# Kernel optimization log

Hardware: AMD Instinct MI355X
Metric: run time of the kernel (lower is better)

Reference implementation:

```python
import jax, jax.numpy as jnp
import numpy as np

IN_DIM = 512
NUM_HEADS = 8
KD = IN_DIM // 2   # 256
VD = IN_DIM        # 512
NEG = -1e9


def setup_inputs() -> dict:
    key = jax.random.key(0)
    k0, k1, k2, k3, k4 = jax.random.split(key, 5)
    B, C, H, W = 2, IN_DIM, 64, 64
    s = lambda fan_in: 1.0 / np.sqrt(fan_in)
    return {
        "X": jax.random.normal(k0, (B, C, H, W), dtype=jnp.float32),
        "Wq": jax.random.normal(k1, (IN_DIM, KD), dtype=jnp.float32) * s(IN_DIM),
        "Wk": jax.random.normal(k2, (IN_DIM, KD), dtype=jnp.float32) * s(IN_DIM),
        "Wv": jax.random.normal(k3, (IN_DIM, VD), dtype=jnp.float32) * s(IN_DIM),
        "Wo": jax.random.normal(k4, (VD, IN_DIM), dtype=jnp.float32) * s(VD),
    }


def reference(X, Wq, Wk, Wv, Wo):
    B, C, H, W = X.shape
    S = H * W
    x = jnp.transpose(X, (0, 2, 3, 1)).reshape(B, S, C)  # [B,S,C]
    dk = KD // NUM_HEADS
    dv = VD // NUM_HEADS
    # projections + head split -> [B,h,S,d]
    q = (x @ Wq).reshape(B, S, NUM_HEADS, dk).transpose(0, 2, 1, 3)
    k = (x @ Wk).reshape(B, S, NUM_HEADS, dk).transpose(0, 2, 1, 3)
    v = (x @ Wv).reshape(B, S, NUM_HEADS, dv).transpose(0, 2, 1, 3)
    q = q * (dk ** -0.5)
    logits = jnp.einsum('bhqd,bhkd->bhqk', q, k)
    bias = NEG * jnp.triu(jnp.ones((S, S), dtype=logits.dtype), 1)  # causal
    weights = jax.nn.softmax(logits + bias, axis=-1)
    out = weights @ v                                  # [B,h,S,dv]
    out = out.transpose(0, 2, 1, 3).reshape(B, S, VD)  # merge heads
    out = out @ Wo
    return out.reshape(B, H, W, C)
```

## Files before the change

### kernel.cpp

```cpp
#include <hip/hip_runtime.h>
#include <hip/hip_bf16.h>
#include <math.h>

#define BATCH 2
#define CH 512
#define SEQ 4096
#define KDIM 256
#define VDIM 512
#define NHEADS 8
#define DK 32
#define DV 64

typedef unsigned short u16;
typedef unsigned int u32;
typedef __attribute__((ext_vector_type(8))) short bf16x8;
typedef __attribute__((ext_vector_type(4))) float f32x4;

__device__ __forceinline__ u16 f2bf(float f) {
    u32 x = __float_as_uint(f);
    u32 r = (x + 0x7fffu + ((x >> 16) & 1u)) >> 16;
    return (u16)r;
}
__device__ __forceinline__ u16 f2bf_fast(float f) {
    return (u16)((__float_as_uint(f) + 0x8000u) >> 16);
}
__device__ __forceinline__ u32 pack2f(float lo, float hi) {
    return (u32)f2bf_fast(lo) | (((__float_as_uint(hi) + 0x8000u) >> 16) << 16);
}

#define QSCALE (0.17677669529663687f * 1.4426950408889634f)


__global__ __launch_bounds__(256) void prep(
    const float* __restrict__ X,
    const float* __restrict__ Wq, const float* __restrict__ Wk,
    const float* __restrict__ Wv, const float* __restrict__ Wo,
    u16* __restrict__ Xb16, u16* __restrict__ Wall, u16* __restrict__ WoT)
{
    __shared__ u16 T[64 * 72];
    const int bid = blockIdx.x;
    const int t = threadIdx.x;
    const int tr = t >> 4;
    const int tc4 = (t & 15) * 4;

    const float* src; u16* dst;
    int src_row0, src_col0, src_pitch, dst_row0, dst_col0, dst_pitch;
    float scale = 1.0f;

    if (bid < 1024) {
        const int b = bid >> 9, rem = bid & 511;
        const int st = rem >> 3, ct = rem & 7;
        src = X + (size_t)b * CH * SEQ;
        src_row0 = ct * 64; src_col0 = st * 64; src_pitch = SEQ;
        dst = Xb16 + (size_t)b * SEQ * CH;
        dst_row0 = st * 64; dst_col0 = ct * 64; dst_pitch = CH;
    } else if (bid < 1152) {
        const int r = bid - 1024;
        const int nt = r >> 3, ct = r & 7;
        if (nt < 4)      { src = Wq; src_col0 = nt * 64;       src_pitch = KDIM; scale = QSCALE; }
        else if (nt < 8) { src = Wk; src_col0 = (nt - 4) * 64; src_pitch = KDIM; }
        else             { src = Wv; src_col0 = (nt - 8) * 64; src_pitch = VDIM; }
        src_row0 = ct * 64;
        dst = Wall; dst_row0 = nt * 64; dst_col0 = ct * 64; dst_pitch = 512;
    } else {
        const int r = bid - 1152;
        const int kt = r >> 3, nt = r & 7;
        src = Wo; src_row0 = kt * 64; src_col0 = nt * 64; src_pitch = 512;
        dst = WoT; dst_row0 = nt * 64; dst_col0 = kt * 64; dst_pitch = 512;
    }

#pragma unroll
    for (int j = 0; j < 4; ++j) {
        const int row = j * 16 + tr;
        const float4 v = *reinterpret_cast<const float4*>(
            &src[(size_t)(src_row0 + row) * src_pitch + src_col0 + tc4]);
        T[(tc4 + 0) * 72 + row] = f2bf(v.x * scale);
        T[(tc4 + 1) * 72 + row] = f2bf(v.y * scale);
        T[(tc4 + 2) * 72 + row] = f2bf(v.z * scale);
        T[(tc4 + 3) * 72 + row] = f2bf(v.w * scale);
    }
    __syncthreads();
#pragma unroll
    for (int j = 0; j < 4; ++j) {
        const int orow = j * 16 + tr;
        const ushort4 o = *reinterpret_cast<ushort4*>(&T[orow * 72 + tc4]);
        *reinterpret_cast<ushort4*>(
            &dst[(size_t)(dst_row0 + orow) * dst_pitch + dst_col0 + tc4]) = o;
    }
}

__global__ __launch_bounds__(256, 2) void qkv3(
    const u16* __restrict__ Xb16, const u16* __restrict__ Wall,
    u16* __restrict__ Qh, u16* __restrict__ Kh, u16* __restrict__ Vh)
{
    __shared__ __align__(16) u16 As[2][128 * 40];
    __shared__ __align__(16) u16 Bs[2][128 * 40];
    const int tid = threadIdx.x;
    const int wv = tid >> 6, lane = tid & 63;
    const int c = lane & 15, quad = lane >> 4;
    const int wm = wv & 1, wn = wv >> 1;
    const int m0 = blockIdx.x * 128;
    const int ny = blockIdx.y;
    const int n0 = ny * 128;

    u16* Y; int N, nbase;
    if (ny < 2)      { Y = Qh; N = KDIM; nbase = 0; }
    else if (ny < 4) { Y = Kh; N = KDIM; nbase = 256; }
    else             { Y = Vh; N = VDIM; nbase = 512; }

    const int srow = tid >> 1, scol = (tid & 1) * 16;

    f32x4 acc[4][4];
#pragma unroll
    for (int i = 0; i < 4; ++i)
#pragma unroll
        for (int g = 0; g < 4; ++g) acc[i][g] = (f32x4){0.f, 0.f, 0.f, 0.f};

    uint4 ar0, ar1, br0, br1;
    auto ld = [&](int k0) {
        const uint4* ap = reinterpret_cast<const uint4*>(
            &Xb16[(size_t)(m0 + srow) * 512 + k0 + scol]);
        ar0 = ap[0]; ar1 = ap[1];
        const uint4* bp = reinterpret_cast<const uint4*>(
            &Wall[(size_t)(n0 + srow) * 512 + k0 + scol]);
        br0 = bp[0]; br1 = bp[1];
    };
    auto stage = [&](int buf) {
        uint4* ad = reinterpret_cast<uint4*>(&As[buf][srow * 40 + scol]);
        ad[0] = ar0; ad[1] = ar1;
        uint4* bd = reinterpret_cast<uint4*>(&Bs[buf][srow * 40 + scol]);
        bd[0] = br0; bd[1] = br1;
    };

    ld(0);
    stage(0);
    ld(32);

    for (int i = 0; i < 16; ++i) {
        const int cur = i & 1;
        __syncthreads();
        stage(cur ^ 1);
        const int k0n = (i + 2 < 16) ? (i + 2) * 32 : 15 * 32;
        ld(k0n);
        bf16x8 af[4], bf_[4];
#pragma unroll
        for (int j = 0; j < 4; ++j) {
            af[j] = *reinterpret_cast<bf16x8*>(
                &As[cur][(wm * 64 + 16 * j + c) * 40 + quad * 8]);
            bf_[j] = *reinterpret_cast<bf16x8*>(
                &Bs[cur][(wn * 64 + 16 * j + c) * 40 + quad * 8]);
        }
#pragma unroll
        for (int j = 0; j < 4; ++j)
#pragma unroll
            for (int g = 0; g < 4; ++g)
                acc[j][g] = __builtin_amdgcn_mfma_f32_16x16x32_bf16(
                    af[j], bf_[g], acc[j][g], 0, 0, 0);
    }
#pragma unroll
    for (int j = 0; j < 4; ++j)
#pragma unroll
        for (int r = 0; r < 4; ++r) {
            const int row = m0 + wm * 64 + 16 * j + quad * 4 + r;
            const int col = n0 - nbase + wn * 64 + c;
#pragma unroll
            for (int g = 0; g < 4; ++g)
                Y[(size_t)row * N + col + 16 * g] = f2bf(acc[j][g][r]);
        }
}

__global__ __launch_bounds__(256, 2) void oproj3(
    const u16* __restrict__ A, const u16* __restrict__ WoT,
    float* __restrict__ Out)
{
    __shared__ __align__(16) u16 As[2][128 * 40];
    __shared__ __align__(16) u16 Bs[2][128 * 40];
    const int tid = threadIdx.x;
    const int wv = tid >> 6, lane = tid & 63;
    const int c = lane & 15, quad = lane >> 4;
    const int wm = wv & 1, wn = wv >> 1;
    const int m0 = blockIdx.x * 128;
    const int n0 = blockIdx.y * 128;

    const int srow = tid >> 1, scol = (tid & 1) * 16;

    f32x4 acc[4][4];
#pragma unroll
    for (int i = 0; i < 4; ++i)
#pragma unroll
        for (int g = 0; g < 4; ++g) acc[i][g] = (f32x4){0.f, 0.f, 0.f, 0.f};

    uint4 ar0, ar1, br0, br1;
    auto ld = [&](int k0) {
        const uint4* ap = reinterpret_cast<const uint4*>(
            &A[(size_t)(m0 + srow) * 512 + k0 + scol]);
        ar0 = ap[0]; ar1 = ap[1];
        const uint4* bp = reinterpret_cast<const uint4*>(
            &WoT[(size_t)(n0 + srow) * 512 + k0 + scol]);
        br0 = bp[0]; br1 = bp[1];
    };
    auto stage = [&](int buf) {
        uint4* ad = reinterpret_cast<uint4*>(&As[buf][srow * 40 + scol]);
        ad[0] = ar0; ad[1] = ar1;
        uint4* bd = reinterpret_cast<uint4*>(&Bs[buf][srow * 40 + scol]);
        bd[0] = br0; bd[1] = br1;
    };

    ld(0);
    stage(0);
    ld(32);

    for (int i = 0; i < 16; ++i) {
        const int cur = i & 1;
        __syncthreads();
        stage(cur ^ 1);
        const int k0n = (i + 2 < 16) ? (i + 2) * 32 : 15 * 32;
        ld(k0n);
        bf16x8 af[4], bf_[4];
#pragma unroll
        for (int j = 0; j < 4; ++j) {
            af[j] = *reinterpret_cast<bf16x8*>(
                &As[cur][(wm * 64 + 16 * j + c) * 40 + quad * 8]);
            bf_[j] = *reinterpret_cast<bf16x8*>(
                &Bs[cur][(wn * 64 + 16 * j + c) * 40 + quad * 8]);
        }
#pragma unroll
        for (int j = 0; j < 4; ++j)
#pragma unroll
            for (int g = 0; g < 4; ++g)
                acc[j][g] = __builtin_amdgcn_mfma_f32_16x16x32_bf16(
                    af[j], bf_[g], acc[j][g], 0, 0, 0);
    }
#pragma unroll
    for (int j = 0; j < 4; ++j)
#pragma unroll
        for (int r = 0; r < 4; ++r) {
            const int row = m0 + wm * 64 + 16 * j + quad * 4 + r;
            const int col = n0 + wn * 64 + c;
#pragma unroll
            for (int g = 0; g < 4; ++g)
                Out[(size_t)row * 512 + col + 16 * g] = acc[j][g][r];
        }
}

__global__ __launch_bounds__(512, 4) void flash_mfma(
    const u16* __restrict__ Q, const u16* __restrict__ K,
    const u16* __restrict__ V, u16* __restrict__ AO)
{
    __shared__ __align__(16) union {
        struct {
            u16 Kl[2][2][64 * 40];
            u16 Vt[2][2][64 * 72];
            u16 Pl[8][16 * 72];
        } t;
        float mg[4][64][40];
    } sh;

    const int tid  = threadIdx.x;
    const int w    = tid >> 6;
    const int ws   = w & 3;
    const int wg   = w >> 2;
    const int lane = tid & 63;
    const int c    = lane & 15;
    const int quad = lane >> 4;
    const int h = blockIdx.y, b = blockIdx.z;

    const int qbA = blockIdx.x;
    const int qbB = 63 - qbA;
    const int q0A = qbA * 64, q0B = qbB * 64;

    const u16* Qb = Q + (size_t)b * SEQ * KDIM + h * DK;
    const u16* Kb = K + (size_t)b * SEQ * KDIM + h * DK;
    const u16* Vb = V + (size_t)b * SEQ * VDIM + h * DV;
    u16* AOb = AO + (size_t)b * SEQ * VDIM + h * DV;

    const bf16x8 qfA = *reinterpret_cast<const bf16x8*>(
        &Qb[(size_t)(q0A + ws * 16 + c) * KDIM + quad * 8]);
    const bf16x8 qfB = *reinterpret_cast<const bf16x8*>(
        &Qb[(size_t)(q0B + ws * 16 + c) * KDIM + quad * 8]);

    const bf16x8 ones = {(short)0x3F80, (short)0x3F80, (short)0x3F80, (short)0x3F80,
                         (short)0x3F80, (short)0x3F80, (short)0x3F80, (short)0x3F80};

    f32x4 oA[4], oB[4];
#pragma unroll
    for (int g = 0; g < 4; ++g) {
        oA[g] = (f32x4){0.f, 0.f, 0.f, 0.f};
        oB[g] = (f32x4){0.f, 0.f, 0.f, 0.f};
    }
    f32x4 laccA = {0.f, 0.f, 0.f, 0.f}, laccB = {0.f, 0.f, 0.f, 0.f};

    const int t256 = tid & 255;
    const int krow = t256 >> 2, kc8 = (t256 & 3) * 8;
    const int vs0 = (t256 & 31) * 2, vd0 = (t256 >> 5) * 8;

    u16* const Plw = sh.t.Pl[w];
    const int T = (qbB >> 1) + 1;

    uint4 kreg, vra, vrb;
    auto ldtile = [&](int kb) {
        const int k0 = kb * 64;
        kreg = *reinterpret_cast<const uint4*>(&Kb[(size_t)(k0 + krow) * KDIM + kc8]);
        vra  = *reinterpret_cast<const uint4*>(&Vb[(size_t)(k0 + vs0) * VDIM + vd0]);
        vrb  = *reinterpret_cast<const uint4*>(&Vb[(size_t)(k0 + vs0 + 1) * VDIM + vd0]);
    };
    auto stagetile = [&](int buf) {
        *reinterpret_cast<uint4*>(&sh.t.Kl[wg][buf][krow * 40 + kc8]) = kreg;
        union { uint4 q; u16 s[8]; } ra, rb;
        ra.q = vra; rb.q = vrb;
#pragma unroll
        for (int i = 0; i < 8; ++i) {
            u32 packed = (u32)ra.s[i] | ((u32)rb.s[i] << 16);
            *reinterpret_cast<u32*>(&sh.t.Vt[wg][buf][(vd0 + i) * 72 + vs0]) = packed;
        }
    };

    ldtile(wg);
    stagetile(0);
    ldtile(2 + wg);

    for (int it = 0; it < T; ++it) {
        const int kb = 2 * it + wg;
        const int k0 = kb * 64;
        const int cur = it & 1;
        __syncthreads();
        stagetile(cur ^ 1);
        {
            int kbn = 2 * (it + 2) + wg; if (kbn > 63) kbn = 63;
            ldtile(kbn);
        }
        const u16* Klc = sh.t.Kl[wg][cur];
        const u16* Vtc = sh.t.Vt[wg][cur];

        auto compute = [&](const bf16x8& qf, int q0, bool diag,
                           f32x4* o, f32x4& lacc) {
            f32x4 s[4];
#pragma unroll
            for (int g = 0; g < 4; ++g) {
                const bf16x8 kf = *reinterpret_cast<const bf16x8*>(
                    &Klc[(c + 16 * g) * 40 + quad * 8]);
                const f32x4 z = {0.f, 0.f, 0.f, 0.f};
                s[g] = __builtin_amdgcn_mfma_f32_16x16x32_bf16(qf, kf, z, 0, 0, 0);
            }
            if (diag) {
#pragma unroll
                for (int g = 0; g < 4; ++g) {
                    const int kcol = k0 + c + 16 * g;
#pragma unroll
                    for (int r = 0; r < 4; ++r) {
                        const int qr = q0 + ws * 16 + quad * 4 + r;
                        if (kcol > qr) s[g][r] = -1e30f;
                    }
                }
            }
#pragma unroll
            for (int g = 0; g < 4; ++g)
#pragma unroll
                for (int r = 0; r < 4; ++r)
                    Plw[(quad * 4 + r) * 72 + c + 16 * g] =
                        f2bf_fast(__builtin_amdgcn_exp2f(s[g][r]));
            const bf16x8 pa0 = *reinterpret_cast<bf16x8*>(&Plw[c * 72 + quad * 8]);
            const bf16x8 pa1 = *reinterpret_cast<bf16x8*>(&Plw[c * 72 + 32 + quad * 8]);
            lacc = __builtin_amdgcn_mfma_f32_16x16x32_bf16(pa0, ones, lacc, 0, 0, 0);
            lacc = __builtin_amdgcn_mfma_f32_16x16x32_bf16(pa1, ones, lacc, 0, 0, 0);
#pragma unroll
            for (int g = 0; g < 4; ++g) {
                const bf16x8 v0 = *reinterpret_cast<const bf16x8*>(
                    &Vtc[(c + 16 * g) * 72 + quad * 8]);
                const bf16x8 v1 = *reinterpret_cast<const bf16x8*>(
                    &Vtc[(c + 16 * g) * 72 + 32 + quad * 8]);
                o[g] = __builtin_amdgcn_mfma_f32_16x16x32_bf16(pa0, v0, o[g], 0, 0, 0);
                o[g] = __builtin_amdgcn_mfma_f32_16x16x32_bf16(pa1, v1, o[g], 0, 0, 0);
            }
        };

        if (kb <= qbA) compute(qfA, q0A, kb == qbA, oA, laccA);
        if (kb <= qbB) compute(qfB, q0B, kb == qbB, oB, laccB);
    }

    __syncthreads();
    if (wg == 1) {
        float* m = sh.mg[ws][lane];
#pragma unroll
        for (int g = 0; g < 4; ++g)
#pragma unroll
            for (int r = 0; r < 4; ++r) {
                m[g * 4 + r]      = oA[g][r];
                m[16 + g * 4 + r] = oB[g][r];
            }
#pragma unroll
        for (int r = 0; r < 4; ++r) { m[32 + r] = laccA[r]; m[36 + r] = laccB[r]; }
    }
    __syncthreads();
    if (wg == 0) {
        const float* m = sh.mg[ws][lane];
#pragma unroll
        for (int g = 0; g < 4; ++g)
#pragma unroll
            for (int r = 0; r < 4; ++r) {
                oA[g][r] += m[g * 4 + r];
                oB[g][r] += m[16 + g * 4 + r];
            }
#pragma unroll
        for (int r = 0; r < 4; ++r) { laccA[r] += m[32 + r]; laccB[r] += m[36 + r]; }
#pragma unroll
        for (int r = 0; r < 4; ++r) {
            const float invA = 1.f / laccA[r];
            const float invB = 1.f / laccB[r];
            const int rowA = q0A + ws * 16 + quad * 4 + r;
            const int rowB = q0B + ws * 16 + quad * 4 + r;
#pragma unroll
            for (int g = 0; g < 4; ++g) {
                AOb[(size_t)rowA * VDIM + c + 16 * g] = f2bf(oA[g][r] * invA);
                AOb[(size_t)rowB * VDIM + c + 16 * g] = f2bf(oB[g][r] * invB);
            }
        }
    }
}

__global__ __launch_bounds__(256) void qkv_proj(
    const float* __restrict__ X,
    const float* __restrict__ Wq, const float* __restrict__ Wk,
    const float* __restrict__ Wv,
    u16* __restrict__ Qh, u16* __restrict__ Kh, u16* __restrict__ Vh)
{
    __shared__ __align__(16) u16 Xs[2][64 * 40];
    __shared__ __align__(16) u16 Wsm[2][64 * 40];
    const int tid = threadIdx.x;
    const int w = tid >> 6, lane = tid & 63;
    const int c = lane & 15, quad = lane >> 4;
    const int s0 = blockIdx.x * 64, b = blockIdx.z;
    const int ny = blockIdx.y;

    const float* Wt; u16* Y; int N, n0; float scale;
    if (ny < 4)       { Wt = Wq; Y = Qh; N = KDIM; n0 = ny * 64;       scale = QSCALE; }
    else if (ny < 8)  { Wt = Wk; Y = Kh; N = KDIM; n0 = (ny - 4) * 64; scale = 1.0f; }
    else              { Wt = Wv; Y = Vh; N = VDIM; n0 = (ny - 8) * 64; scale = 1.0f; }

    const float* Xb = X + (size_t)b * CH * SEQ;
    const int cp = tid >> 4;
    const int s4 = (tid & 15) * 4;

    f32x4 acc[4];
#pragma unroll
    for (int g = 0; g < 4; ++g) acc[g] = (f32x4){0.f, 0.f, 0.f, 0.f};

    auto ldx = [&](int c0, float4& a, float4& bb) {
        a  = *reinterpret_cast<const float4*>(&Xb[(size_t)(c0 + 2 * cp) * SEQ + s0 + s4]);
        bb = *reinterpret_cast<const float4*>(&Xb[(size_t)(c0 + 2 * cp + 1) * SEQ + s0 + s4]);
    };
    auto ldwf = [&](int c0, float4& a, float4& bb) {
        a  = *reinterpret_cast<const float4*>(&Wt[(size_t)(c0 + 2 * cp) * N + n0 + s4]);
        bb = *reinterpret_cast<const float4*>(&Wt[(size_t)(c0 + 2 * cp + 1) * N + n0 + s4]);
    };
    auto stage = [&](int buf, const float4& xa, const float4& xb,
                     const float4& wa, const float4& wb) {
        const float a[4] = {xa.x, xa.y, xa.z, xa.w};
        const float bb[4] = {xb.x, xb.y, xb.z, xb.w};
        const float aw[4] = {wa.x, wa.y, wa.z, wa.w};
        const float bw[4] = {wb.x, wb.y, wb.z, wb.w};
#pragma unroll
        for (int i = 0; i < 4; ++i) {
            *reinterpret_cast<u32*>(&Xs[buf][(s4 + i) * 40 + 2 * cp]) = pack2f(a[i], bb[i]);
            *reinterpret_cast<u32*>(&Wsm[buf][(s4 + i) * 40 + 2 * cp]) = pack2f(aw[i], bw[i]);
        }
    };

    float4 xa, xb, wa, wb;
    ldx(0, xa, xb); ldwf(0, wa, wb);
    stage(0, xa, xb, wa, wb);
    ldx(32, xa, xb); ldwf(32, wa, wb);

    for (int i = 0; i < 16; ++i) {
        const int cur = i & 1;
        __syncthreads();
        stage(cur ^ 1, xa, xb, wa, wb);
        const int c0n = (i + 2 < 16) ? (i + 2) * 32 : 15 * 32;
        ldx(c0n, xa, xb); ldwf(c0n, wa, wb);
        const bf16x8 af = *reinterpret_cast<bf16x8*>(&Xs[cur][(w * 16 + c) * 40 + quad * 8]);
#pragma unroll
        for (int g = 0; g < 4; ++g) {
            bf16x8 bf_ = *reinterpret_cast<bf16x8*>(&Wsm[cur][(c + 16 * g) * 40 + quad * 8]);
            acc[g] = __builtin_amdgcn_mfma_f32_16x16x32_bf16(af, bf_, acc[g], 0, 0, 0);
        }
    }
    u16* Yb = Y + (size_t)b * SEQ * N;
#pragma unroll
    for (int r = 0; r < 4; ++r) {
        const int row = s0 + w * 16 + quad * 4 + r;
#pragma unroll
        for (int g = 0; g < 4; ++g)
            Yb[(size_t)row * N + n0 + c + 16 * g] = f2bf(acc[g][r] * scale);
    }
}

__global__ __launch_bounds__(256) void oproj_mfma(
    const u16* __restrict__ A, const float* __restrict__ Wo,
    float* __restrict__ Out)
{
    __shared__ __align__(16) u16 Ws[2][64 * 40];
    const int tid = threadIdx.x;
    const int w = tid >> 6, lane = tid & 63;
    const int c = lane & 15, quad = lane >> 4;
    const int m0 = blockIdx.x * 64, n0 = blockIdx.y * 64;
    const int kp = tid >> 4;
    const int n4 = (tid & 15) * 4;
    const u16* Arow = &A[(size_t)(m0 + w * 16 + c) * 512];

    f32x4 acc[4];
#pragma unroll
    for (int g = 0; g < 4; ++g) acc[g] = (f32x4){0.f, 0.f, 0.f, 0.f};

    auto ldwf = [&](int k0, float4& a, float4& bb) {
        a  = *reinterpret_cast<const float4*>(&Wo[(size_t)(k0 + 2 * kp) * 512 + n0 + n4]);
        bb = *reinterpret_cast<const float4*>(&Wo[(size_t)(k0 + 2 * kp + 1) * 512 + n0 + n4]);
    };
    auto stage = [&](int buf, const float4& wa, const float4& wb) {
        const float a[4] = {wa.x, wa.y, wa.z, wa.w};
        const float bb[4] = {wb.x, wb.y, wb.z, wb.w};
#pragma unroll
        for (int i = 0; i < 4; ++i)
            *reinterpret_cast<u32*>(&Ws[buf][(n4 + i) * 40 + 2 * kp]) = pack2f(a[i], bb[i]);
    };

    float4 wa, wb;
    ldwf(0, wa, wb);
    stage(0, wa, wb);
    ldwf(32, wa, wb);
    bf16x8 afc = *reinterpret_cast<const bf16x8*>(&Arow[quad * 8]);

    for (int i = 0; i < 16; ++i) {
        const int cur = i & 1;
        __syncthreads();
        stage(cur ^ 1, wa, wb);
        const int k0n = (i + 2 < 16) ? (i + 2) * 32 : 15 * 32;
        ldwf(k0n, wa, wb);
        const int k0a = (i + 1 < 16) ? (i + 1) * 32 : 15 * 32;
        const bf16x8 afn = *reinterpret_cast<const bf16x8*>(&Arow[k0a + quad * 8]);
#pragma unroll
        for (int g = 0; g < 4; ++g) {
            bf16x8 bf_ = *reinterpret_cast<bf16x8*>(&Ws[cur][(c + 16 * g) * 40 + quad * 8]);
            acc[g] = __builtin_amdgcn_mfma_f32_16x16x32_bf16(afc, bf_, acc[g], 0, 0, 0);
        }
        afc = afn;
    }
#pragma unroll
    for (int r = 0; r < 4; ++r) {
        const int row = m0 + w * 16 + quad * 4 + r;
#pragma unroll
        for (int g = 0; g < 4; ++g)
            Out[(size_t)row * 512 + n0 + c + 16 * g] = acc[g][r];
    }
}

extern "C" void kernel_launch(void* const* d_in, const int* in_sizes, int n_in,
                              void* d_out, int out_size, void* d_ws, size_t ws_size,
                              hipStream_t stream) {
    const float* X  = (const float*)d_in[0];
    const float* Wq = (const float*)d_in[1];
    const float* Wk = (const float*)d_in[2];
    const float* Wv = (const float*)d_in[3];
    const float* Wo = (const float*)d_in[4];
    float* out = (float*)d_out;

    const size_t qk = (size_t)BATCH * SEQ * KDIM;
    const size_t vs = (size_t)BATCH * SEQ * VDIM;
    u16* Qh  = (u16*)d_ws;
    u16* Kh  = Qh + qk;
    u16* Vh  = Kh + qk;
    u16* XA  = Vh + vs;
    u16* Wall = XA + vs;
    u16* WoT  = Wall + 1024 * 512;
    const size_t need_fast = (size_t)(WoT + 512 * 512 - (u16*)d_ws) * sizeof(u16);

    if (ws_size >= need_fast) {
        prep<<<dim3(1216), 256, 0, stream>>>(X, Wq, Wk, Wv, Wo, XA, Wall, WoT);
        qkv3<<<dim3((BATCH * SEQ) / 128, 8), 256, 0, stream>>>(XA, Wall, Qh, Kh, Vh);
        flash_mfma<<<dim3(32, NHEADS, BATCH), 512, 0, stream>>>(Qh, Kh, Vh, XA);
        oproj3<<<dim3((BATCH * SEQ) / 128, 4), 256, 0, stream>>>(XA, WoT, out);
    } else {
        u16* AOh = XA;
        qkv_proj<<<dim3(SEQ / 64, 16, BATCH), 256, 0, stream>>>(
            X, Wq, Wk, Wv, Qh, Kh, Vh);
        flash_mfma<<<dim3(32, NHEADS, BATCH), 512, 0, stream>>>(Qh, Kh, Vh, AOh);
        oproj_mfma<<<dim3((BATCH * SEQ) / 64, VDIM / 64), 256, 0, stream>>>(AOh, Wo, out);
    }
}
```

Baseline: 159.8 us.

## Transpose attention MFMAs and pass P via permlane swaps instead of LDS

Swaps the MFMA operand order so S and O come out transposed (keys/values along rows), which lets each lane hold P values in the layout needed as the B operand of the PV MFMA. The exponentiated scores are packed with v_cvt_pk_bf16_f32 and rearranged across lanes with permlane32/permlane16 swaps, removing the per-warp LDS P buffer and its write/read round trip. The epilogue now writes four contiguous bf16 outputs per store and uses a single row-sum value per lane. This relies on gfx950 permlane intrinsics and a correct lane mapping, and it shrinks LDS usage, which may allow more occupancy.

Measured after the change: 152.3 us. 4.7% less time.

```diff
diff --git a/kernel.cpp b/kernel.cpp
--- a/kernel.cpp
+++ b/kernel.cpp
@@ -26,6 +26,11 @@
 }
 __device__ __forceinline__ u32 pack2f(float lo, float hi) {
     return (u32)f2bf_fast(lo) | (((__float_as_uint(hi) + 0x8000u) >> 16) << 16);
+}
+__device__ __forceinline__ u32 cvtpk_bf16(float lo, float hi) {
+    u32 r;
+    asm("v_cvt_pk_bf16_f32 %0, %1, %2" : "=v"(r) : "v"(lo), "v"(hi));
+    return r;
 }
 
 #define QSCALE (0.17677669529663687f * 1.4426950408889634f)
@@ -251,7 +256,6 @@
         struct {
             u16 Kl[2][2][64 * 40];
             u16 Vt[2][2][64 * 72];
-            u16 Pl[8][16 * 72];
         } t;
         float mg[4][64][40];
     } sh;
@@ -294,7 +298,7 @@
     const int krow = t256 >> 2, kc8 = (t256 & 3) * 8;
     const int vs0 = (t256 & 31) * 2, vd0 = (t256 >> 5) * 8;
 
-    u16* const Plw = sh.t.Pl[w];
+    const int qrbase = ws * 16 + c;
     const int T = (qbB >> 1) + 1;
 
     uint4 kreg, vra, vrb;
@@ -340,37 +344,57 @@
                 const bf16x8 kf = *reinterpret_cast<const bf16x8*>(
                     &Klc[(c + 16 * g) * 40 + quad * 8]);
                 const f32x4 z = {0.f, 0.f, 0.f, 0.f};
-                s[g] = __builtin_amdgcn_mfma_f32_16x16x32_bf16(qf, kf, z, 0, 0, 0);
+                s[g] = __builtin_amdgcn_mfma_f32_16x16x32_bf16(kf, qf, z, 0, 0, 0);
             }
             if (diag) {
+                const int qr = q0 + qrbase;
 #pragma unroll
                 for (int g = 0; g < 4; ++g) {
-                    const int kcol = k0 + c + 16 * g;
-#pragma unroll
-                    for (int r = 0; r < 4; ++r) {
-                        const int qr = q0 + ws * 16 + quad * 4 + r;
-                        if (kcol > qr) s[g][r] = -1e30f;
-                    }
+                    const int kc0 = k0 + 16 * g + quad * 4;
+#pragma unroll
+                    for (int r = 0; r < 4; ++r)
+                        if (kc0 + r > qr) s[g][r] = -1e30f;
                 }
             }
+            u32 wk[4][2];
 #pragma unroll
             for (int g = 0; g < 4; ++g)
 #pragma unroll
-                for (int r = 0; r < 4; ++r)
-                    Plw[(quad * 4 + r) * 72 + c + 16 * g] =
-                        f2bf_fast(__builtin_amdgcn_exp2f(s[g][r]));
-            const bf16x8 pa0 = *reinterpret_cast<bf16x8*>(&Plw[c * 72 + quad * 8]);
-            const bf16x8 pa1 = *reinterpret_cast<bf16x8*>(&Plw[c * 72 + 32 + quad * 8]);
-            lacc = __builtin_amdgcn_mfma_f32_16x16x32_bf16(pa0, ones, lacc, 0, 0, 0);
-            lacc = __builtin_amdgcn_mfma_f32_16x16x32_bf16(pa1, ones, lacc, 0, 0, 0);
+                for (int j2 = 0; j2 < 2; ++j2)
+                    wk[g][j2] = cvtpk_bf16(
+                        __builtin_amdgcn_exp2f(s[g][2 * j2]),
+                        __builtin_amdgcn_exp2f(s[g][2 * j2 + 1]));
+            union { u32 wq[4]; bf16x8 v; } ub0, ub1;
+#pragma unroll
+            for (int j2 = 0; j2 < 2; ++j2) {
+                {
+                    auto t1 = __builtin_amdgcn_permlane32_swap(
+                        wk[0][j2], wk[1][j2], false, false);
+                    auto t2 = __builtin_amdgcn_permlane16_swap(
+                        (u32)t1[0], (u32)t1[1], false, false);
+                    ub0.wq[j2]     = (u32)t2[0];
+                    ub0.wq[2 + j2] = (u32)t2[1];
+                }
+                {
+                    auto t1 = __builtin_amdgcn_permlane32_swap(
+                        wk[2][j2], wk[3][j2], false, false);
+                    auto t2 = __builtin_amdgcn_permlane16_swap(
+                        (u32)t1[0], (u32)t1[1], false, false);
+                    ub1.wq[j2]     = (u32)t2[0];
+                    ub1.wq[2 + j2] = (u32)t2[1];
+                }
+            }
+            const bf16x8 pb0 = ub0.v, pb1 = ub1.v;
+            lacc = __builtin_amdgcn_mfma_f32_16x16x32_bf16(ones, pb0, lacc, 0, 0, 0);
+            lacc = __builtin_amdgcn_mfma_f32_16x16x32_bf16(ones, pb1, lacc, 0, 0, 0);
 #pragma unroll
             for (int g = 0; g < 4; ++g) {
                 const bf16x8 v0 = *reinterpret_cast<const bf16x8*>(
                     &Vtc[(c + 16 * g) * 72 + quad * 8]);
                 const bf16x8 v1 = *reinterpret_cast<const bf16x8*>(
                     &Vtc[(c + 16 * g) * 72 + 32 + quad * 8]);
-                o[g] = __builtin_amdgcn_mfma_f32_16x16x32_bf16(pa0, v0, o[g], 0, 0, 0);
-                o[g] = __builtin_amdgcn_mfma_f32_16x16x32_bf16(pa1, v1, o[g], 0, 0, 0);
+                o[g] = __builtin_amdgcn_mfma_f32_16x16x32_bf16(v0, pb0, o[g], 0, 0, 0);
+                o[g] = __builtin_amdgcn_mfma_f32_16x16x32_bf16(v1, pb1, o[g], 0, 0, 0);
             }
         };
 
@@ -388,8 +412,8 @@
                 m[g * 4 + r]      = oA[g][r];
                 m[16 + g * 4 + r] = oB[g][r];
             }
-#pragma unroll
-        for (int r = 0; r < 4; ++r) { m[32 + r] = laccA[r]; m[36 + r] = laccB[r]; }
+        m[32] = laccA[0];
+        m[33] = laccB[0];
     }
     __syncthreads();
     if (wg == 0) {
@@ -401,19 +425,21 @@
                 oA[g][r] += m[g * 4 + r];
                 oB[g][r] += m[16 + g * 4 + r];
             }
-#pragma unroll
-        for (int r = 0; r < 4; ++r) { laccA[r] += m[32 + r]; laccB[r] += m[36 + r]; }
-#pragma unroll
-        for (int r = 0; r < 4; ++r) {
-            const float invA = 1.f / laccA[r];
-            const float invB = 1.f / laccB[r];
-            const int rowA = q0A + ws * 16 + quad * 4 + r;
-            const int rowB = q0B + ws * 16 + quad * 4 + r;
-#pragma unroll
-            for (int g = 0; g < 4; ++g) {
-                AOb[(size_t)rowA * VDIM + c + 16 * g] = f2bf(oA[g][r] * invA);
-                AOb[(size_t)rowB * VDIM + c + 16 * g] = f2bf(oB[g][r] * invB);
-            }
+        const float invA = 1.f / (laccA[0] + m[32]);
+        const float invB = 1.f / (laccB[0] + m[33]);
+        const int rowA = q0A + qrbase;
+        const int rowB = q0B + qrbase;
+#pragma unroll
+        for (int g = 0; g < 4; ++g) {
+            ushort4 a4, b4;
+            a4.x = f2bf(oA[g][0] * invA); a4.y = f2bf(oA[g][1] * invA);
+            a4.z = f2bf(oA[g][2] * invA); a4.w = f2bf(oA[g][3] * invA);
+            b4.x = f2bf(oB[g][0] * invB); b4.y = f2bf(oB[g][1] * invB);
+            b4.z = f2bf(oB[g][2] * invB); b4.w = f2bf(oB[g][3] * invB);
+            *reinterpret_cast<ushort4*>(
+                &AOb[(size_t)rowA * VDIM + 16 * g + quad * 4]) = a4;
+            *reinterpret_cast<ushort4*>(
+                &AOb[(size_t)rowB * VDIM + 16 * g + quad * 4]) = b4;
         }
     }
 }
```
